# Performance work log

Hardware: AMD Instinct MI355X
Metric: run time of the kernel (lower is better)

Reference implementation:

```python
import jax, jax.numpy as jnp
import numpy as np

N = 96                       # max_num_nodes
T = N * (N + 1) // 2         # upper-triangular vector length
E = 256                      # embedding_dim
MAX_ITERS = 50


def setup_inputs() -> dict:
    key = jax.random.key(0)
    ks = jax.random.split(key, 8)
    graph_embedding = jax.random.normal(ks[0], (1, E), jnp.float32)
    a = (jax.random.uniform(ks[1], (1, N, N)) < 0.1).astype(jnp.float32)
    adj = jnp.maximum(a, jnp.swapaxes(a, 1, 2))  # symmetric 0/1 adjacency
    mask = jnp.ones((1, N), bool)
    W1 = jax.random.normal(ks[2], (E, 250), jnp.float32) * 0.08
    b1 = jnp.zeros((250,), jnp.float32)
    W2 = jax.random.normal(ks[3], (250, 100), jnp.float32) * 0.10
    b2 = jnp.zeros((100,), jnp.float32)
    W3 = jax.random.normal(ks[4], (100, T), jnp.float32) * 0.15
    b3 = jnp.zeros((T,), jnp.float32)
    return dict(graph_embedding=graph_embedding, adj=adj, mask=mask,
                W1=W1, b1=b1, W2=W2, b2=b2, W3=W3, b3=b3)


def _forward(graph_embedding, adj, mask, W1, b1, W2, b2, W3, b3):
    idx = jnp.arange(N)
    eye = jnp.eye(N, dtype=adj.dtype)

    # decoder: Linear -> Linear -> ReLU -> Linear -> sigmoid
    h = graph_embedding @ W1 + b1
    h = jax.nn.relu(h @ W2 + b2)
    l = jax.nn.sigmoid(h @ W3 + b3)[0]              # [T]

    # recover_adj_lower + recover_full_adj_from_lower
    iu = jnp.triu_indices(N)
    up = jnp.zeros((N, N), l.dtype).at[iu].set(l)    # row-major triu fill, as torch bool-mask assign
    recon = up + up.T - jnp.diag(jnp.diag(up))       # [N, N]
    fr = recon.sum(axis=1)                           # recon degree features

    # ori_adj with diagonal forced to 1 where mask
    a0 = adj[0]
    m = mask[0]
    ori = a0.at[idx, idx].set(jnp.where(m, jnp.asarray(1.0, a0.dtype), jnp.diag(a0)))
    f = ori.sum(axis=1)                              # ori degree features

    # edge_similarity_matrix, vectorized
    # off-diagonal block: S[i,j,a,b] = A[i,j]A[i,i]A[j,j] * R[a,b]R[a,a]R[b,b]  (i!=j, a!=b)
    dA = jnp.diag(ori)
    dR = jnp.diag(recon)
    t1 = (1.0 - eye) * ori * dA[:, None] * dA[None, :]      # [N, N], zero on diag
    t2 = (1.0 - eye) * recon * dR[:, None] * dR[None, :]    # [N, N], zero on diag
    S = t1[:, :, None, None] * t2[None, None, :, :]          # [N, N, N, N]
    # diagonal block: S[i,i,a,a] = A[i,i]R[a,a] / (|f_i - fr_a| + 1)
    sim = 1.0 / (jnp.abs(f[:, None] - fr[None, :]) + 1.0)    # [N, N]
    D = dA[:, None] * dR[None, :] * sim                      # [N, N]
    S = S.at[idx[:, None], idx[:, None], idx[None, :], idx[None, :]].set(D)

    # mpm: iterative max-pooling matching
    x0 = jnp.full((N, N), 1.0 / N, dtype=S.dtype)
    off_mask = (1.0 - eye)[:, :, None]                       # exclude j == i

    def step(x, _):
        pooled = jnp.max(x[None, :, None, :] * S, axis=3)    # [i, j, a] = max_b x[j,b]*S[i,j,a,b]
        neigh = (off_mask * pooled).sum(axis=1)              # [i, a]
        x_new = x * D + neigh                                # D[i,a] == S[i,i,a,a]
        x_new = x_new / jnp.linalg.norm(x_new)
        return x_new, None

    x, _ = jax.lax.scan(step, x0, None, length=MAX_ITERS)
    return x  # soft assignment matrix [N, N]


def reference(graph_embedding, adj, mask, W1, b1, W2, b2, W3, b3):
    return _forward(graph_embedding, adj, mask, W1, b1, W2, b2, W3, b3)
```

## Files before the change

kernel.cpp:

```cpp
#include <hip/hip_runtime.h>
#include <hip/hip_bf16.h>

#define NN 96
#define NB 32
#define NTH 256
#define RPB 3
#define OPA 144
#define NITER 50
#define SMASK 0x8000000080000000ULL
#define SPIN_MAX 32768
#define MAXF 32

typedef unsigned long long ull;
typedef float v2f __attribute__((ext_vector_type(2)));

__device__ __forceinline__ float bf2f(__hip_bfloat16 v){ return __bfloat162float(v); }
__device__ __forceinline__ float LD(const void* p, int i, bool f32){
  return f32 ? ((const float*)p)[i]
             : __bfloat162float(((const __hip_bfloat16*)p)[i]);
}
__device__ __forceinline__ float ldA(const float* p){
  return __hip_atomic_load(p, __ATOMIC_RELAXED, __HIP_MEMORY_SCOPE_AGENT);
}
__device__ __forceinline__ void stA(float* p, float v){
  __hip_atomic_store(p, v, __ATOMIC_RELAXED, __HIP_MEMORY_SCOPE_AGENT);
}
__device__ __forceinline__ ull ldA64(const ull* p){
  return __hip_atomic_load(p, __ATOMIC_RELAXED, __HIP_MEMORY_SCOPE_AGENT);
}
__device__ __forceinline__ void stA64(ull* p, ull v){
  __hip_atomic_store(p, v, __ATOMIC_RELAXED, __HIP_MEMORY_SCOPE_AGENT);
}

__global__ __launch_bounds__(NTH, 1) void gvae(
    const void* __restrict__ ge,  const void* __restrict__ adj,
    const void* __restrict__ W1,  const void* __restrict__ b1,
    const void* __restrict__ W2,  const void* __restrict__ b2,
    const void* __restrict__ W3,  const void* __restrict__ b3,
    void* __restrict__ out, float* __restrict__ ws)
{
  __shared__ __align__(16) float t2s[NN * NN + 1400];
  __shared__ __align__(16) float Ms[NN * NN];
  __shared__ __align__(16) float xs[RPB * NN];
  __shared__ __align__(16) float Ds[RPB * NN];
  __shared__ float ges[256], h1s[250], h2s[100];
  __shared__ unsigned char nbl[RPB * 96];
  __shared__ unsigned char onbl[RPB * 2];
  __shared__ int   fcnts[RPB], ocnts[RPB];
  __shared__ float fdeg[RPB];
  __shared__ float frs[NN], dRs[NN];
  __shared__ float wred[4];
  __shared__ float s_sh;
  __shared__ int   bdone;

  const int tid = threadIdx.x, blk = blockIdx.x;

  float* pn  = ws;
  float* lg  = ws + 2048;
  ull*   Mb0 = (ull*)(ws + 8192);
  ull*   Mb1 = Mb0 + 4608;

  if (blk >= NB){
    if (tid == 0) bdone = 0;
    __syncthreads();
    const float* dn = ws + 1664;
    const int wv = tid >> 6;
    float a0 = 1.1f + blk, a1 = 2.2f, a2 = 3.3f, a3 = 4.4f;
    float a4 = 5.5f, a5 = 6.6f, a6 = 7.7f, a7 = 8.8f;
    const float m = 1.0000001f;
    for (int outer = 0; outer < 16384; ++outer){
#pragma unroll
      for (int u = 0; u < 2; ++u){
        a0 = fmaf(a0, m, 1e-6f); a1 = fmaf(a1, m, 2e-6f);
        a2 = fmaf(a2, m, 3e-6f); a3 = fmaf(a3, m, 4e-6f);
        a4 = fmaf(a4, m, 5e-6f); a5 = fmaf(a5, m, 6e-6f);
        a6 = fmaf(a6, m, 7e-6f); a7 = fmaf(a7, m, 8e-6f);
      }
      __builtin_amdgcn_s_sleep(4);
      int stop;
      if (wv == 0){
        float v = (tid == 0 && (outer & 7) == 0) ? ldA(dn) : 0.f;
        stop = __any(v > 0.5f) ? 1 : 0;
        if (stop && tid == 0)
          __hip_atomic_store(&bdone, 1, __ATOMIC_RELAXED, __HIP_MEMORY_SCOPE_WORKGROUP);
      } else {
        stop = __hip_atomic_load(&bdone, __ATOMIC_RELAXED, __HIP_MEMORY_SCOPE_WORKGROUP);
      }
      if (stop) break;
    }
    float sum = a0 + a1 + a2 + a3 + a4 + a5 + a6 + a7;
    if (sum == 0.12345678f) stA(ws + 1700, sum);
    return;
  }

  float sv = (tid < 128) ? bf2f(((const __hip_bfloat16*)W1)[tid])
                         : bf2f(((const __hip_bfloat16*)W3)[tid - 128]);
  const bool isf32 = __syncthreads_or(!(fabsf(sv) < 1e4f)) != 0;

  if (tid < 256) ges[tid] = LD(ge, tid, isf32);
  __syncthreads();
  if (tid < 250){
    float a0 = LD(b1, tid, isf32), a1 = 0.f, a2 = 0.f, a3 = 0.f;
    for (int e = 0; e < 256; e += 4){
      a0 += ges[e]     * LD(W1, (e    ) * 250 + tid, isf32);
      a1 += ges[e + 1] * LD(W1, (e + 1) * 250 + tid, isf32);
      a2 += ges[e + 2] * LD(W1, (e + 2) * 250 + tid, isf32);
      a3 += ges[e + 3] * LD(W1, (e + 3) * 250 + tid, isf32);
    }
    h1s[tid] = (a0 + a1) + (a2 + a3);
  }
  __syncthreads();
  if (tid < 100){
    float a0 = LD(b2, tid, isf32), a1 = 0.f;
    for (int k = 0; k < 250; k += 2){
      a0 += h1s[k]     * LD(W2, (k    ) * 100 + tid, isf32);
      a1 += h1s[k + 1] * LD(W2, (k + 1) * 100 + tid, isf32);
    }
    h2s[tid] = fmaxf(a0 + a1, 0.f);
  }
  __syncthreads();

  if (tid < 146){
    int o = blk * 146 + tid;
    if (o < 4656){
      float a = LD(b3, o, isf32);
      for (int k = 0; k < 100; ++k) a += h2s[k] * LD(W3, k * 4656 + o, isf32);
      stA(&lg[o], 1.f / (1.f + expf(-a)));
    }
  }
  if (tid >= 192 && tid < 192 + RPB){
    int r = tid - 192, ig = blk * RPB + r;
    int lo = blk * RPB, hi = lo + RPB;
    float fs = 1.f; int c = 0, co = 0;
    for (int j = 0; j < NN; ++j){
      if (j == ig) continue;
      float v = LD(adj, ig * NN + j, isf32);
      fs += v;
      if (v > 0.5f){
        if (j >= lo && j < hi) onbl[r * 2 + (co++)] = (unsigned char)j;
        else                   nbl[r * 96 + (c++)]  = (unsigned char)j;
      }
    }
    fcnts[r] = c; ocnts[r] = co; fdeg[r] = fs;
  }
  {
    float vv[19];
    unsigned pend = 0;
#pragma unroll
    for (int c = 0; c < 19; ++c) if (tid + NTH * c < 4656) pend |= 1u << c;
    int spin = 0;
    while (pend && spin++ < SPIN_MAX){
      unsigned p2 = pend;
#pragma unroll
      for (int c = 0; c < 19; ++c)
        if ((p2 >> c) & 1) vv[c] = ldA(&lg[tid + NTH * c]);
#pragma unroll
      for (int c = 0; c < 19; ++c)
        if (((p2 >> c) & 1) && vv[c] > 0.f){
          Ms[tid + NTH * c] = vv[c];
          pend &= ~(1u << c);
        }
      if (pend == p2) __builtin_amdgcn_s_sleep(2);
    }
  }
  __syncthreads();

  for (int e = tid; e < NN * NN; e += NTH){
    int a = e / NN, b = e % NN, i = min(a, b), j = max(a, b);
    int k = i * NN - (i * (i - 1)) / 2 + (j - i);
    t2s[e] = Ms[k];
  }
  __syncthreads();
  if (tid < NN){
    float srow = 0.f;
    for (int b = 0; b < NN; ++b) srow += t2s[b * NN + tid];
    frs[tid] = srow; dRs[tid] = t2s[tid * NN + tid];
  }
  __syncthreads();
  for (int e = tid; e < NN * NN; e += NTH){
    int a = e / NN, b = e % NN;
    t2s[e] = (a == b) ? 0.f : t2s[e] * dRs[a] * dRs[b];
  }
  for (int o = tid; o < RPB * NN; o += NTH){
    int r = o / NN, a = o % NN;
    Ds[o] = dRs[a] / (fabsf(fdeg[r] - frs[a]) + 1.f);
    xs[o] = 1.f / 96.f;
  }
  __syncthreads();

  int r = 0, p = 0, nf = 0, fc = 0, oc = 0, gw = 0;
  int off[MAXF]; int oad0 = 0, oad1 = 0;
  if (tid < OPA){
    r = tid / 48; p = tid - r * 48;
    fc = fcnts[r]; oc = ocnts[r];
    nf = fc < MAXF ? fc : MAXF;
    gw = (blk * RPB + r) * 48 + p;
#pragma unroll
    for (int c = 0; c < MAXF; ++c)
      off[c] = (c < nf) ? ((int)nbl[r * 96 + c] * 48 + p) : gw;
    oad0 = (oc > 0) ? ((int)onbl[r * 2]     * NN + 2 * p) : 0;
    oad1 = (oc > 1) ? ((int)onbl[r * 2 + 1] * NN + 2 * p) : 0;
  }

  for (int it = 0; it < NITER; ++it){
    ull* Mw = (it & 1) ? Mb1 : Mb0;
    const ull sg = ((it >> 1) & 1) ? SMASK : 0ULL;

    if (tid == 0 && it > 0){
      float t = (wred[0] + wred[1]) + (wred[2] + wred[3]);
      stA(&pn[it * NB + blk], t);
    }

    if (tid < OPA){
      v2f m0 = {0.f, 0.f}, m1 = {0.f, 0.f};
      for (int b = 0; b < NN; b += 2){
        v2f t0 = *(const v2f*)&t2s[(b    ) * NN + 2 * p];
        v2f t1 = *(const v2f*)&t2s[(b + 1) * NN + 2 * p];
        v2f xv = *(const v2f*)&xs[r * NN + b];
        m0.x = fmaxf(m0.x, xv.x * t0.x); m0.y = fmaxf(m0.y, xv.x * t0.y);
        m1.x = fmaxf(m1.x, xv.y * t1.x); m1.y = fmaxf(m1.y, xv.y * t1.y);
      }
      float mx = fmaxf(m0.x, m1.x), my = fmaxf(m0.y, m1.y);
      *(v2f*)&Ms[(blk * RPB + r) * NN + 2 * p] = (v2f){mx, my};
      ull enc = (((ull)__float_as_uint(my + 1.f)) << 32) | __float_as_uint(mx + 1.f);
      stA64(&Mw[gw], enc ^ sg);
    } else if (tid >= 192 && it >= 2){
      int pt = tid - 192;
      float v = 0.f;
      if (pt < NB){
        int sp = 0;
        for (;;){
          v = ldA(&pn[(it - 1) * NB + pt]);
          if (v > 0.f || ++sp >= SPIN_MAX) break;
          __builtin_amdgcn_s_sleep(1);
        }
      }
      for (int o2 = 16; o2; o2 >>= 1) v += __shfl_down(v, o2, 64);
      if (pt == 0) s_sh = rsqrtf(v);
    }
    __syncthreads();

    float s = (it < 2) ? 1.f : s_sh;
    float nsq = 0.f;
    if (tid < OPA){
      ull vv[MAXF];
      unsigned pend = (nf >= 32) ? 0xffffffffu : ((1u << nf) - 1u);
      int spin = 0;
      while (pend && spin++ < SPIN_MAX){
        unsigned p2 = pend;
#pragma unroll
        for (int c = 0; c < MAXF; ++c)
          if ((p2 >> c) & 1) vv[c] = ldA64(&Mw[off[c]]);
#pragma unroll
        for (int c = 0; c < MAXF; ++c)
          if (((p2 >> c) & 1) && !((vv[c] ^ sg) & SMASK)) pend &= ~(1u << c);
      }
      v2f acc = {0.f, 0.f};
#pragma unroll
      for (int c = 0; c < MAXF; ++c)
        if (c < nf){
          acc.x += fabsf(__uint_as_float((unsigned)vv[c])) - 1.f;
          acc.y += fabsf(__uint_as_float((unsigned)(vv[c] >> 32))) - 1.f;
        }
      for (int c = MAXF; c < fc; ++c){
        int o3 = (int)nbl[r * 96 + c] * 48 + p;
        ull w; int sp = 0;
        do { w = ldA64(&Mw[o3]); } while (((w ^ sg) & SMASK) && ++sp < SPIN_MAX);
        acc.x += fabsf(__uint_as_float((unsigned)w)) - 1.f;
        acc.y += fabsf(__uint_as_float((unsigned)(w >> 32))) - 1.f;
      }
      if (oc > 0){ v2f mv = *(const v2f*)&Ms[oad0]; acc.x += mv.x; acc.y += mv.y; }
      if (oc > 1){ v2f mv = *(const v2f*)&Ms[oad1]; acc.x += mv.x; acc.y += mv.y; }
      v2f w2 = *(const v2f*)&xs[r * NN + 2 * p];
      v2f d2 = *(const v2f*)&Ds[r * NN + 2 * p];
      v2f u; u.x = s * (w2.x * d2.x + acc.x); u.y = s * (w2.y * d2.y + acc.y);
      *(v2f*)&xs[r * NN + 2 * p] = u;
      nsq = u.x * u.x + u.y * u.y;
    }
    for (int o2 = 32; o2; o2 >>= 1) nsq += __shfl_down(nsq, o2, 64);
    if ((tid & 63) == 0) wred[tid >> 6] = nsq;
    __syncthreads();
  }

  if (tid == 0){
    float t = (wred[0] + wred[1]) + (wred[2] + wred[3]);
    stA(&pn[NITER * NB + blk], t);
  }
  if (tid < NB){
    float v; int sp = 0;
    for (;;){
      v = ldA(&pn[NITER * NB + tid]);
      if (v > 0.f || ++sp >= SPIN_MAX) break;
      __builtin_amdgcn_s_sleep(1);
    }
    for (int o2 = 16; o2; o2 >>= 1) v += __shfl_down(v, o2, 64);
    if (tid == 0) s_sh = rsqrtf(v);
  }
  __syncthreads();
  float sf = s_sh;
  for (int o = tid; o < RPB * NN; o += NTH){
    int og = blk * RPB * NN + o;
    float v = sf * xs[o];
    if (isf32) ((float*)out)[og] = v;
    else       ((__hip_bfloat16*)out)[og] = __float2bfloat16(v);
  }
  if (blk == 0 && tid == 0) stA(ws + 1664, 1.f);
}

extern "C" void kernel_launch(void* const* d_in, const int* in_sizes, int n_in,
                              void* d_out, int out_size, void* d_ws, size_t ws_size,
                              hipStream_t stream) {
  (void)in_sizes; (void)n_in; (void)out_size; (void)ws_size;
  hipLaunchKernelGGL(gvae, dim3(256), dim3(NTH), 0, stream,
                     d_in[0], d_in[1], d_in[3], d_in[4], d_in[5], d_in[6],
                     d_in[7], d_in[8], d_out, (float*)d_ws);
}
```

Before: 456.6 us.

## Replace per-iteration block barriers with wave-level stamp-based producer/consumer sync

Each of the three row waves now runs its own iteration loop, and the fourth wave becomes a dedicated norm-reduction and global-sum service. Per-iteration __syncthreads are replaced by LDS stamps with acquire/release semantics and ring buffers for row maxima, partial norms and scale factors. The aim is to remove block-wide barrier stalls and let waves progress independently across iterations. In exchange the code is more complex, and ordering or spin-timeout bugs could break correctness.

```diff
diff --git a/kernel.cpp b/kernel.cpp
--- a/kernel.cpp
+++ b/kernel.cpp
@@ -5,7 +5,6 @@
 #define NB 32
 #define NTH 256
 #define RPB 3
-#define OPA 144
 #define NITER 50
 #define SMASK 0x8000000080000000ULL
 #define SPIN_MAX 32768
@@ -30,6 +29,12 @@
 }
 __device__ __forceinline__ void stA64(ull* p, ull v){
   __hip_atomic_store(p, v, __ATOMIC_RELAXED, __HIP_MEMORY_SCOPE_AGENT);
+}
+__device__ __forceinline__ int ldSacq(const int* p){
+  return __hip_atomic_load(p, __ATOMIC_ACQUIRE, __HIP_MEMORY_SCOPE_WORKGROUP);
+}
+__device__ __forceinline__ void stSrel(int* p, int v){
+  __hip_atomic_store(p, v, __ATOMIC_RELEASE, __HIP_MEMORY_SCOPE_WORKGROUP);
 }
 
 __global__ __launch_bounds__(NTH, 1) void gvae(
@@ -39,18 +44,22 @@
     const void* __restrict__ W3,  const void* __restrict__ b3,
     void* __restrict__ out, float* __restrict__ ws)
 {
-  __shared__ __align__(16) float t2s[NN * NN + 1400];
-  __shared__ __align__(16) float Ms[NN * NN];
+  __shared__ __align__(16) float t2s[NN * NN + 4600];
+  __shared__ __align__(16) float stg[4656];
   __shared__ __align__(16) float xs[RPB * NN];
   __shared__ __align__(16) float Ds[RPB * NN];
+  __shared__ __align__(16) float msd[4 * RPB * NN];
   __shared__ float ges[256], h1s[250], h2s[100];
   __shared__ unsigned char nbl[RPB * 96];
   __shared__ unsigned char onbl[RPB * 2];
   __shared__ int   fcnts[RPB], ocnts[RPB];
   __shared__ float fdeg[RPB];
   __shared__ float frs[NN], dRs[NN];
-  __shared__ float wred[4];
-  __shared__ float s_sh;
+  __shared__ float wpart[4 * RPB];
+  __shared__ int   wpstamp[4 * RPB];
+  __shared__ int   rstamp[4 * RPB];
+  __shared__ float sring[8];
+  __shared__ int   sstamp[8];
   __shared__ int   bdone;
 
   const int tid = threadIdx.x, blk = blockIdx.x;
@@ -137,7 +146,7 @@
       float v = LD(adj, ig * NN + j, isf32);
       fs += v;
       if (v > 0.5f){
-        if (j >= lo && j < hi) onbl[r * 2 + (co++)] = (unsigned char)j;
+        if (j >= lo && j < hi) onbl[r * 2 + (co++)] = (unsigned char)(j - lo);
         else                   nbl[r * 96 + (c++)]  = (unsigned char)j;
       }
     }
@@ -157,7 +166,7 @@
 #pragma unroll
       for (int c = 0; c < 19; ++c)
         if (((p2 >> c) & 1) && vv[c] > 0.f){
-          Ms[tid + NTH * c] = vv[c];
+          stg[tid + NTH * c] = vv[c];
           pend &= ~(1u << c);
         }
       if (pend == p2) __builtin_amdgcn_s_sleep(2);
@@ -168,7 +177,7 @@
   for (int e = tid; e < NN * NN; e += NTH){
     int a = e / NN, b = e % NN, i = min(a, b), j = max(a, b);
     int k = i * NN - (i * (i - 1)) / 2 + (j - i);
-    t2s[e] = Ms[k];
+    t2s[e] = stg[k];
   }
   __syncthreads();
   if (tid < NN){
@@ -186,118 +195,146 @@
     Ds[o] = dRs[a] / (fabsf(fdeg[r] - frs[a]) + 1.f);
     xs[o] = 1.f / 96.f;
   }
-  __syncthreads();
-
-  int r = 0, p = 0, nf = 0, fc = 0, oc = 0, gw = 0;
-  int off[MAXF]; int oad0 = 0, oad1 = 0;
-  if (tid < OPA){
-    r = tid / 48; p = tid - r * 48;
-    fc = fcnts[r]; oc = ocnts[r];
-    nf = fc < MAXF ? fc : MAXF;
-    gw = (blk * RPB + r) * 48 + p;
-#pragma unroll
-    for (int c = 0; c < MAXF; ++c)
-      off[c] = (c < nf) ? ((int)nbl[r * 96 + c] * 48 + p) : gw;
-    oad0 = (oc > 0) ? ((int)onbl[r * 2]     * NN + 2 * p) : 0;
-    oad1 = (oc > 1) ? ((int)onbl[r * 2 + 1] * NN + 2 * p) : 0;
-  }
-
-  for (int it = 0; it < NITER; ++it){
-    ull* Mw = (it & 1) ? Mb1 : Mb0;
-    const ull sg = ((it >> 1) & 1) ? SMASK : 0ULL;
-
-    if (tid == 0 && it > 0){
-      float t = (wred[0] + wred[1]) + (wred[2] + wred[3]);
-      stA(&pn[it * NB + blk], t);
-    }
-
-    if (tid < OPA){
-      v2f m0 = {0.f, 0.f}, m1 = {0.f, 0.f};
-      for (int b = 0; b < NN; b += 2){
-        v2f t0 = *(const v2f*)&t2s[(b    ) * NN + 2 * p];
-        v2f t1 = *(const v2f*)&t2s[(b + 1) * NN + 2 * p];
-        v2f xv = *(const v2f*)&xs[r * NN + b];
-        m0.x = fmaxf(m0.x, xv.x * t0.x); m0.y = fmaxf(m0.y, xv.x * t0.y);
-        m1.x = fmaxf(m1.x, xv.y * t1.x); m1.y = fmaxf(m1.y, xv.y * t1.y);
-      }
-      float mx = fmaxf(m0.x, m1.x), my = fmaxf(m0.y, m1.y);
-      *(v2f*)&Ms[(blk * RPB + r) * NN + 2 * p] = (v2f){mx, my};
-      ull enc = (((ull)__float_as_uint(my + 1.f)) << 32) | __float_as_uint(mx + 1.f);
-      stA64(&Mw[gw], enc ^ sg);
-    } else if (tid >= 192 && it >= 2){
-      int pt = tid - 192;
-      float v = 0.f;
-      if (pt < NB){
-        int sp = 0;
-        for (;;){
-          v = ldA(&pn[(it - 1) * NB + pt]);
-          if (v > 0.f || ++sp >= SPIN_MAX) break;
-          __builtin_amdgcn_s_sleep(1);
-        }
-      }
-      for (int o2 = 16; o2; o2 >>= 1) v += __shfl_down(v, o2, 64);
-      if (pt == 0) s_sh = rsqrtf(v);
-    }
-    __syncthreads();
-
-    float s = (it < 2) ? 1.f : s_sh;
-    float nsq = 0.f;
-    if (tid < OPA){
-      ull vv[MAXF];
-      unsigned pend = (nf >= 32) ? 0xffffffffu : ((1u << nf) - 1u);
-      int spin = 0;
-      while (pend && spin++ < SPIN_MAX){
-        unsigned p2 = pend;
+  if (tid < 4 * RPB){ rstamp[tid] = -1; wpstamp[tid] = -1; }
+  if (tid < 8) sstamp[tid] = -1;
+  __syncthreads();
+
+  const int wv = tid >> 6, l = tid & 63;
+
+  if (wv < RPB){
+    const int g = blk * RPB + wv;
+    const bool act = (l < 48);
+    const int p = l;
+    int fc = 0, nf = 0, gw = 0;
+    int off[MAXF];
+    const int oc  = ocnts[wv];
+    const int ow0 = onbl[wv * 2], ow1 = onbl[wv * 2 + 1];
+    if (act){
+      fc = fcnts[wv]; nf = fc < MAXF ? fc : MAXF;
+      gw = g * 48 + p;
+#pragma unroll
+      for (int c = 0; c < MAXF; ++c)
+        off[c] = (c < nf) ? ((int)nbl[wv * 96 + c] * 48 + p) : gw;
+    }
+
+    for (int it = 0; it < NITER; ++it){
+      ull* Mw = (it & 1) ? Mb1 : Mb0;
+      const ull sg = ((it >> 1) & 1) ? SMASK : 0ULL;
+      const int ring = (it & 3) * RPB;
+
+      float mx = 0.f, my = 0.f;
+      if (act){
+        v2f m0 = {0.f, 0.f}, m1 = {0.f, 0.f};
+        for (int b = 0; b < NN; b += 2){
+          v2f t0 = *(const v2f*)&t2s[(b    ) * NN + 2 * p];
+          v2f t1 = *(const v2f*)&t2s[(b + 1) * NN + 2 * p];
+          v2f xv = *(const v2f*)&xs[wv * NN + b];
+          m0.x = fmaxf(m0.x, xv.x * t0.x); m0.y = fmaxf(m0.y, xv.x * t0.y);
+          m1.x = fmaxf(m1.x, xv.y * t1.x); m1.y = fmaxf(m1.y, xv.y * t1.y);
+        }
+        mx = fmaxf(m0.x, m1.x); my = fmaxf(m0.y, m1.y);
+        *(v2f*)&msd[(ring + wv) * NN + 2 * p] = (v2f){mx, my};
+      }
+      if (l == 0) stSrel(&rstamp[ring + wv], it);
+      if (act){
+        ull enc = (((ull)__float_as_uint(my + 1.f)) << 32) | __float_as_uint(mx + 1.f);
+        stA64(&Mw[gw], enc ^ sg);
+      }
+
+      float s = 1.f;
+      if (it >= 2){
+        int sl = it & 7, sp = 0;
+        while (ldSacq(&sstamp[sl]) != it && ++sp < SPIN_MAX)
+          if ((sp & 63) == 0) __builtin_amdgcn_s_sleep(1);
+        s = sring[sl];
+      }
+
+      v2f acc = {0.f, 0.f};
+      if (act){
+        ull vv[MAXF];
+        unsigned pend = (nf >= 32) ? 0xffffffffu : ((1u << nf) - 1u);
+        int spin = 0;
+        while (pend && spin++ < SPIN_MAX){
+          unsigned p2 = pend;
+#pragma unroll
+          for (int c = 0; c < MAXF; ++c)
+            if ((p2 >> c) & 1) vv[c] = ldA64(&Mw[off[c]]);
+#pragma unroll
+          for (int c = 0; c < MAXF; ++c)
+            if (((p2 >> c) & 1) && !((vv[c] ^ sg) & SMASK)) pend &= ~(1u << c);
+        }
 #pragma unroll
         for (int c = 0; c < MAXF; ++c)
-          if ((p2 >> c) & 1) vv[c] = ldA64(&Mw[off[c]]);
-#pragma unroll
-        for (int c = 0; c < MAXF; ++c)
-          if (((p2 >> c) & 1) && !((vv[c] ^ sg) & SMASK)) pend &= ~(1u << c);
-      }
-      v2f acc = {0.f, 0.f};
-#pragma unroll
-      for (int c = 0; c < MAXF; ++c)
-        if (c < nf){
-          acc.x += fabsf(__uint_as_float((unsigned)vv[c])) - 1.f;
-          acc.y += fabsf(__uint_as_float((unsigned)(vv[c] >> 32))) - 1.f;
-        }
-      for (int c = MAXF; c < fc; ++c){
-        int o3 = (int)nbl[r * 96 + c] * 48 + p;
-        ull w; int sp = 0;
-        do { w = ldA64(&Mw[o3]); } while (((w ^ sg) & SMASK) && ++sp < SPIN_MAX);
-        acc.x += fabsf(__uint_as_float((unsigned)w)) - 1.f;
-        acc.y += fabsf(__uint_as_float((unsigned)(w >> 32))) - 1.f;
-      }
-      if (oc > 0){ v2f mv = *(const v2f*)&Ms[oad0]; acc.x += mv.x; acc.y += mv.y; }
-      if (oc > 1){ v2f mv = *(const v2f*)&Ms[oad1]; acc.x += mv.x; acc.y += mv.y; }
-      v2f w2 = *(const v2f*)&xs[r * NN + 2 * p];
-      v2f d2 = *(const v2f*)&Ds[r * NN + 2 * p];
-      v2f u; u.x = s * (w2.x * d2.x + acc.x); u.y = s * (w2.y * d2.y + acc.y);
-      *(v2f*)&xs[r * NN + 2 * p] = u;
-      nsq = u.x * u.x + u.y * u.y;
-    }
-    for (int o2 = 32; o2; o2 >>= 1) nsq += __shfl_down(nsq, o2, 64);
-    if ((tid & 63) == 0) wred[tid >> 6] = nsq;
-    __syncthreads();
-  }
-
-  if (tid == 0){
-    float t = (wred[0] + wred[1]) + (wred[2] + wred[3]);
-    stA(&pn[NITER * NB + blk], t);
-  }
-  if (tid < NB){
-    float v; int sp = 0;
-    for (;;){
-      v = ldA(&pn[NITER * NB + tid]);
-      if (v > 0.f || ++sp >= SPIN_MAX) break;
-      __builtin_amdgcn_s_sleep(1);
-    }
-    for (int o2 = 16; o2; o2 >>= 1) v += __shfl_down(v, o2, 64);
-    if (tid == 0) s_sh = rsqrtf(v);
-  }
-  __syncthreads();
-  float sf = s_sh;
+          if (c < nf){
+            acc.x += fabsf(__uint_as_float((unsigned)vv[c])) - 1.f;
+            acc.y += fabsf(__uint_as_float((unsigned)(vv[c] >> 32))) - 1.f;
+          }
+        for (int c = MAXF; c < fc; ++c){
+          int o3 = (int)nbl[wv * 96 + c] * 48 + p;
+          ull w; int sp = 0;
+          do { w = ldA64(&Mw[o3]); } while (((w ^ sg) & SMASK) && ++sp < SPIN_MAX);
+          acc.x += fabsf(__uint_as_float((unsigned)w)) - 1.f;
+          acc.y += fabsf(__uint_as_float((unsigned)(w >> 32))) - 1.f;
+        }
+      }
+      for (int t = 0; t < oc; ++t){
+        int wj = (t == 0) ? ow0 : ow1;
+        int rs = ring + wj, sp = 0;
+        while (ldSacq(&rstamp[rs]) != it && ++sp < SPIN_MAX){}
+        if (act){
+          v2f mv = *(const v2f*)&msd[rs * NN + 2 * p];
+          acc.x += mv.x; acc.y += mv.y;
+        }
+      }
+
+      float nsq = 0.f;
+      if (act){
+        v2f w2 = *(const v2f*)&xs[wv * NN + 2 * p];
+        v2f d2 = *(const v2f*)&Ds[wv * NN + 2 * p];
+        v2f u; u.x = s * (w2.x * d2.x + acc.x); u.y = s * (w2.y * d2.y + acc.y);
+        *(v2f*)&xs[wv * NN + 2 * p] = u;
+        nsq = u.x * u.x + u.y * u.y;
+      }
+      for (int o2 = 32; o2; o2 >>= 1) nsq += __shfl_down(nsq, o2, 64);
+      if (l == 0){
+        wpart[ring + wv] = nsq;
+        stSrel(&wpstamp[ring + wv], it);
+      }
+    }
+  } else {
+    for (int it = 0; it <= NITER; ++it){
+      if (l == 0 && it >= 1){
+        int sl = ((it - 1) & 3) * RPB; float t = 0.f;
+        for (int w = 0; w < RPB; ++w){
+          int sp = 0;
+          while (ldSacq(&wpstamp[sl + w]) != it - 1 && ++sp < SPIN_MAX)
+            if ((sp & 63) == 0) __builtin_amdgcn_s_sleep(1);
+          t += wpart[sl + w];
+        }
+        stA(&pn[it * NB + blk], t);
+      }
+      if (it >= 2){
+        int slot = (it == NITER) ? NITER : (it - 1);
+        float v = 0.f;
+        if (l < NB){
+          int sp = 0;
+          for (;;){
+            v = ldA(&pn[slot * NB + l]);
+            if (v > 0.f || ++sp >= SPIN_MAX) break;
+            __builtin_amdgcn_s_sleep(1);
+          }
+        }
+        for (int o2 = 16; o2; o2 >>= 1) v += __shfl_down(v, o2, 64);
+        if (l == 0){
+          sring[it & 7] = rsqrtf(v);
+          stSrel(&sstamp[it & 7], it);
+        }
+      }
+    }
+  }
+  __syncthreads();
+
+  float sf = sring[NITER & 7];
   for (int o = tid; o < RPB * NN; o += NTH){
     int og = blk * RPB * NN + o;
     float v = sf * xs[o];
```

Result: faster. 402.1 us (-11.9%).
